# Performance work log

Measured on AMD Instinct MI355X. Metric: run time of the kernel, lower is better.

Reference implementation:

```python
import jax, jax.numpy as jnp
import numpy as np

MIN_NEAR = 0.05
DENSITY_SCALE = 1.0
BOUND = 1.0  # spherical scene bounds radius
GEO = 15


def _density_mlp(x, dW1, db1, dW2, db2, dW3, db3):
    h = jax.nn.relu(x @ dW1 + db1)
    h = jax.nn.relu(h @ dW2 + db2)
    h = h @ dW3 + db3  # [M, 1+GEO]
    sigma = jnp.exp(jnp.clip(h[..., 0], -15.0, 15.0))  # trunc_exp
    return sigma, h[..., 1:]


def _color_mlp(d, geo, cW1, cb1, cW2, cb2, cW3, cb3):
    h = jnp.concatenate([d, geo], axis=-1)
    h = jax.nn.relu(h @ cW1 + cb1)
    h = jax.nn.relu(h @ cW2 + cb2)
    return jax.nn.sigmoid(h @ cW3 + cb3)


def _comp_weights(deltas, sigmas):
    # alpha compositing: w_i = alpha_i * prod_{j<i}(1 - alpha_j)
    alphas = 1.0 - jnp.exp(-deltas * sigmas)
    trans = jnp.cumprod(
        jnp.concatenate([jnp.ones_like(alphas[:, :1]), 1.0 - alphas + 1e-15], axis=-1),
        axis=-1)[:, :-1]
    return alphas * trans


def _sample_pdf(bins, weights, n_samples):
    # deterministic importance resampling (eval mode); bins [N,T-1], weights [N,T-2]
    weights = weights + 1e-5
    pdf = weights / jnp.sum(weights, axis=-1, keepdims=True)
    cdf = jnp.cumsum(pdf, axis=-1)
    cdf = jnp.concatenate([jnp.zeros_like(cdf[:, :1]), cdf], axis=-1)  # [N, T-1]
    u = jnp.linspace(0.5 / n_samples, 1.0 - 0.5 / n_samples, n_samples)
    u = jnp.broadcast_to(u, (bins.shape[0], n_samples))
    inds = jax.vmap(lambda c, uu: jnp.searchsorted(c, uu, side='right'))(cdf, u)
    below = jnp.clip(inds - 1, 0, cdf.shape[-1] - 1)
    above = jnp.clip(inds, 0, cdf.shape[-1] - 1)
    cdf_g0 = jnp.take_along_axis(cdf, below, axis=-1)
    cdf_g1 = jnp.take_along_axis(cdf, above, axis=-1)
    bmax = bins.shape[-1] - 1
    bins_g0 = jnp.take_along_axis(bins, jnp.clip(below, 0, bmax), axis=-1)
    bins_g1 = jnp.take_along_axis(bins, jnp.clip(above, 0, bmax), axis=-1)
    denom = jnp.where(cdf_g1 - cdf_g0 < 1e-5, 1.0, cdf_g1 - cdf_g0)
    t = (u - cdf_g0) / denom
    return bins_g0 + t * (bins_g1 - bins_g0)


def _run(rays_o, rays_d, dW1, db1, dW2, db2, dW3, db3,
         cW1, cb1, cW2, cb2, cW3, cb3, num_steps, upsample_steps):
    N = rays_o.shape[0]
    # get_z_val_bounds: ray/sphere intersection, sphere radius BOUND at origin
    b = jnp.sum(rays_o * rays_d, axis=-1)
    c = jnp.sum(rays_o * rays_o, axis=-1) - BOUND ** 2
    disc = jnp.maximum(b * b - c, 0.0)
    z_max = jnp.maximum(-b + jnp.sqrt(disc), MIN_NEAR + 1e-3)
    z_min = jnp.full_like(z_max, MIN_NEAR)
    # get_foreground_z_vals: per-ray linspace (perturb=False)
    t = jnp.linspace(0.0, 1.0, num_steps)
    z_vals = z_min[:, None] + (z_max - z_min)[:, None] * t[None, :]
    z_vals = jnp.clip(z_vals, z_min[:, None], z_max[:, None])
    xyzs = rays_o[:, None, :] + rays_d[:, None, :] * z_vals[..., None]
    sigma, geo = _density_mlp(xyzs.reshape(-1, 3), dW1, db1, dW2, db2, dW3, db3)
    sigma = sigma.reshape(N, num_steps)
    geo = geo.reshape(N, num_steps, GEO)

    # upsample_z_values: importance resampling from coarse weights
    deltas = z_vals[:, 1:] - z_vals[:, :-1]
    aug = jnp.concatenate([deltas, deltas[:, -1:]], axis=-1)
    w_coarse = _comp_weights(aug, DENSITY_SCALE * sigma)
    z_mid = 0.5 * (z_vals[:, :-1] + z_vals[:, 1:])
    new_z = jax.lax.stop_gradient(_sample_pdf(z_mid, w_coarse[:, 1:-1], upsample_steps))
    new_xyzs = rays_o[:, None, :] + rays_d[:, None, :] * new_z[..., None]
    new_sigma, new_geo = _density_mlp(new_xyzs.reshape(-1, 3), dW1, db1, dW2, db2, dW3, db3)
    new_sigma = new_sigma.reshape(N, upsample_steps)
    new_geo = new_geo.reshape(N, upsample_steps, GEO)

    # sort/gather merge of coarse + fine samples
    z_all = jnp.concatenate([z_vals, new_z], axis=1)
    order = jnp.argsort(z_all, axis=1)
    z_vals = jnp.take_along_axis(z_all, order, axis=1)  # [N, T]
    xyzs = jnp.take_along_axis(jnp.concatenate([xyzs, new_xyzs], axis=1), order[..., None], axis=1)
    sigma = jnp.take_along_axis(jnp.concatenate([sigma, new_sigma], axis=1), order, axis=1)
    geo = jnp.take_along_axis(jnp.concatenate([geo, new_geo], axis=1), order[..., None], axis=1)

    deltas = z_vals[:, 1:] - z_vals[:, :-1]
    aug = jnp.concatenate([deltas, deltas[:, -1:]], axis=-1)
    weights = _comp_weights(aug, DENSITY_SCALE * sigma)  # [N, T]

    mask = weights > 1e-4
    dirs = jnp.broadcast_to(rays_d[:, None, :], xyzs.shape).reshape(-1, 3)
    rgb = _color_mlp(dirs, geo.reshape(-1, GEO), cW1, cb1, cW2, cb2, cW3, cb3)
    rgbs = jnp.where(mask.reshape(-1, 1), rgb, 0.0).reshape(N, -1, 3)

    weights_sum = jnp.sum(weights, axis=-1)
    depth = jnp.sum(weights * z_vals, axis=-1)
    image = jnp.sum(weights[..., None] * rgbs, axis=-2)
    bg = 206.0 / 255.0
    image = image + (1.0 - weights_sum)[..., None] * bg

    # pairwise distortion loss (the (z_shifted - z_shifted) term in the source is identically zero)
    sample_dist = 1.0 / num_steps
    z_shift = jnp.concatenate([z_vals[:, 1:], jnp.full((N, 1), sample_dist, z_vals.dtype)], axis=-1)
    mid_zs = 0.5 * z_vals + 0.5 * z_shift
    pair = jnp.abs(mid_zs[:, None, :] - mid_zs[:, :, None]) * (weights[:, None, :] * weights[:, :, None])
    loss = jnp.sum(pair, axis=(1, 2)) / (depth + 1e-6)
    loss = jnp.where(loss < 1e-3, 0.0, loss)  # cutoff
    return jnp.concatenate([image, depth[:, None], loss[:, None]], axis=-1)  # [N, 5]


def setup_inputs() -> dict:
    key = jax.random.key(0)
    ks = jax.random.split(key, 16)
    N, H = 2048, 256
    rays_o = 0.1 * jax.random.normal(ks[0], (N, 3), jnp.float32)  # near scene centre
    rd = jax.random.normal(ks[1], (N, 3), jnp.float32)
    rays_d = rd / jnp.linalg.norm(rd, axis=-1, keepdims=True)

    def w(k, shape):
        return jax.random.normal(k, shape, jnp.float32) * (1.0 / np.sqrt(shape[0]))

    return {
        'rays_o': rays_o, 'rays_d': rays_d,
        'dW1': w(ks[2], (3, H)), 'db1': jnp.zeros(H, jnp.float32),
        'dW2': w(ks[3], (H, H)), 'db2': jnp.zeros(H, jnp.float32),
        'dW3': w(ks[4], (H, 1 + GEO)), 'db3': jnp.zeros(1 + GEO, jnp.float32),
        'cW1': w(ks[5], (3 + GEO, H)), 'cb1': jnp.zeros(H, jnp.float32),
        'cW2': w(ks[6], (H, H)), 'cb2': jnp.zeros(H, jnp.float32),
        'cW3': w(ks[7], (H, 3)), 'cb3': jnp.zeros(3, jnp.float32),
        'num_steps': 128, 'upsample_steps': 128,
    }


def reference(rays_o, rays_d, dW1, db1, dW2, db2, dW3, db3,
              cW1, cb1, cW2, cb2, cW3, cb3, num_steps, upsample_steps):
    return _run(rays_o, rays_d, dW1, db1, dW2, db2, dW3, db3,
                cW1, cb1, cW2, cb2, cW3, cb3, num_steps, upsample_steps)
```

## Files before the change

### kernel.cpp

```cpp
#include <hip/hip_runtime.h>


typedef float f32x4 __attribute__((ext_vector_type(4)));
typedef __bf16 bf16x8 __attribute__((ext_vector_type(8)));
typedef __bf16 bf16x4 __attribute__((ext_vector_type(4)));
typedef unsigned short u16x8 __attribute__((ext_vector_type(8)));
typedef unsigned short u16x4 __attribute__((ext_vector_type(4)));

#define NRAYS 2048
#define NSTEP 128
#define MIN_NEAR 0.05f

#define OFF_D1 0
#define OFF_D2 8192
#define OFF_D3 73728
#define OFF_C1 77824
#define OFF_C2 86016
#define OFF_C3 151552
#define PACK_TOTAL 155648

__device__ __forceinline__ unsigned short f2bf(float f) {
  __bf16 h = (__bf16)f;
  return __builtin_bit_cast(unsigned short, h);
}
__device__ __forceinline__ u16x4 pack4(float a, float b, float c, float d) {
  bf16x4 h;
  h[0] = (__bf16)a; h[1] = (__bf16)b; h[2] = (__bf16)c; h[3] = (__bf16)d;
  return __builtin_bit_cast(u16x4, h);
}

__device__ __forceinline__ float ray_zmax(const float* __restrict__ ro,
                                          const float* __restrict__ rd, int r) {
  float ox = ro[r * 3], oy = ro[r * 3 + 1], oz = ro[r * 3 + 2];
  float dx = rd[r * 3], dy = rd[r * 3 + 1], dz = rd[r * 3 + 2];
  float b = ox * dx + oy * dy + oz * dz;
  float c = ox * ox + oy * oy + oz * oz - 1.0f;
  float disc = fmaxf(b * b - c, 0.0f);
  return fmaxf(-b + sqrtf(disc), MIN_NEAR + 1e-3f);
}
__device__ __forceinline__ float z_at(float zmax, int i) {
  float zz = MIN_NEAR + (zmax - MIN_NEAR) * ((float)i / 127.0f);
  return fminf(fmaxf(zz, MIN_NEAR), zmax);
}

__device__ __forceinline__ float wave_iscan(float v, int lane) {
#pragma unroll
  for (int off = 1; off < 64; off <<= 1) {
    float y = __shfl_up(v, off, 64);
    if (lane >= off) v += y;
  }
  return v;
}
__device__ __forceinline__ float block_iscan(float v, float* part, int lane, int wid) {
  float s = wave_iscan(v, lane);
  if (lane == 63) part[wid] = s;
  __syncthreads();
  float pre = 0.f;
  if (wid > 0) pre += part[0];
  if (wid > 1) pre += part[1];
  if (wid > 2) pre += part[2];
  return s + pre;
}

__device__ __forceinline__ void pack_std(const float* __restrict__ W,
                                         unsigned short* __restrict__ dst,
                                         int idx, int K, int Norig, int NT) {
  int per = NT * 512;
  int kt = idx / per, rm = idx % per;
  int nt = rm >> 9, lane = (rm >> 3) & 63, j = rm & 7;
  int k = kt * 32 + ((lane >> 4) << 3) + j;
  int n = nt * 16 + (lane & 15);
  float v = (k < K && n < Norig) ? W[k * Norig + n] : 0.0f;
  dst[idx] = f2bf(v);
}

__global__ void k_pack_all(const float* __restrict__ dW1, const float* __restrict__ dW2,
                           const float* __restrict__ dW3, const float* __restrict__ cW1,
                           const float* __restrict__ cW2, const float* __restrict__ cW3,
                           unsigned short* __restrict__ Wp) {
  int idx = blockIdx.x * 256 + threadIdx.x;
  if (idx < OFF_D2) {
    pack_std(dW1, Wp + OFF_D1, idx - OFF_D1, 3, 256, 16);
  } else if (idx < OFF_D3) {
    pack_std(dW2, Wp + OFF_D2, idx - OFF_D2, 256, 256, 16);
  } else if (idx < OFF_C1) {
    int j2 = idx - OFF_D3;
    int lane = (j2 >> 3) & 63, jj = j2 & 7, kt = j2 >> 9;
    int k = kt * 32 + ((lane >> 4) << 3) + jj;
    int n = lane & 15;
    Wp[idx] = f2bf(dW3[k * 16 + ((n + 1) & 15)]);
  } else if (idx < OFF_C2) {
    int j2 = idx - OFF_C1;
    int nt = j2 >> 9, lane = (j2 >> 3) & 63, jj = j2 & 7;
    int k = ((lane >> 4) << 3) + jj;
    int n = nt * 16 + (lane & 15);
    float v = 0.0f;
    if (k < 15) v = cW1[(3 + k) * 256 + n];
    else if (k >= 16 && k < 19) v = cW1[(k - 16) * 256 + n];
    Wp[idx] = f2bf(v);
  } else if (idx < OFF_C3) {
    pack_std(cW2, Wp + OFF_C2, idx - OFF_C2, 256, 256, 16);
  } else if (idx < PACK_TOTAL) {
    pack_std(cW3, Wp + OFF_C3, idx - OFF_C3, 256, 3, 1);
  }
}


__device__ __forceinline__ void mlp_l1(const unsigned short* xb, unsigned short* dst,
                                       const bf16x8 (&w1r)[4], const float* sb1,
                                       int wid, int quad, int col) {
#pragma unroll
  for (int h = 0; h < 2; ++h) {
    f32x4 acc[8];
#pragma unroll
    for (int i = 0; i < 8; ++i) acc[i] = (f32x4){0.f, 0.f, 0.f, 0.f};
    int p0 = (h * 2) * 16 + col, p1 = (h * 2 + 1) * 16 + col;
    bf16x8 x0 = *reinterpret_cast<const bf16x8*>(&xb[p0 * 32 + ((quad ^ (p0 & 3)) * 8)]);
    bf16x8 x1 = *reinterpret_cast<const bf16x8*>(&xb[p1 * 32 + ((quad ^ (p1 & 3)) * 8)]);
#pragma unroll
    for (int ntl = 0; ntl < 4; ++ntl) {
      acc[ntl * 2 + 0] = __builtin_amdgcn_mfma_f32_16x16x32_bf16(w1r[ntl], x0, acc[ntl * 2 + 0], 0, 0, 0);
      acc[ntl * 2 + 1] = __builtin_amdgcn_mfma_f32_16x16x32_bf16(w1r[ntl], x1, acc[ntl * 2 + 1], 0, 0, 0);
    }
#pragma unroll
    for (int ntl = 0; ntl < 4; ++ntl) {
      int n = (wid * 4 + ntl) * 16 + quad * 4;
      f32x4 bv = *reinterpret_cast<const f32x4*>(&sb1[n]);
#pragma unroll
      for (int j = 0; j < 2; ++j) {
        int p = (h * 2 + j) * 16 + col;
        *reinterpret_cast<u16x4*>(&dst[p * 256 + (((n >> 3) ^ (p & 31)) * 8) + (n & 7)]) =
            pack4(fmaxf(acc[ntl * 2 + j][0] + bv[0], 0.f), fmaxf(acc[ntl * 2 + j][1] + bv[1], 0.f),
                  fmaxf(acc[ntl * 2 + j][2] + bv[2], 0.f), fmaxf(acc[ntl * 2 + j][3] + bv[3], 0.f));
      }
    }
  }
}

__device__ __forceinline__ void l2_pass(const unsigned short* src, unsigned short* dst,
                                        const bf16x8 (&w2r)[8][4], const float* sb2,
                                        int h, int wid, int quad, int col) {
  f32x4 acc[8];
#pragma unroll
  for (int i = 0; i < 8; ++i) acc[i] = (f32x4){0.f, 0.f, 0.f, 0.f};
  const int p0 = (h * 2) * 16 + col, p1 = (h * 2 + 1) * 16 + col;
#pragma unroll
  for (int kt = 0; kt < 8; ++kt) {
    bf16x8 x0 = *reinterpret_cast<const bf16x8*>(&src[p0 * 256 + (((kt * 4 + quad) ^ (p0 & 31)) * 8)]);
    bf16x8 x1 = *reinterpret_cast<const bf16x8*>(&src[p1 * 256 + (((kt * 4 + quad) ^ (p1 & 31)) * 8)]);
#pragma unroll
    for (int ntl = 0; ntl < 4; ++ntl) {
      acc[ntl * 2 + 0] = __builtin_amdgcn_mfma_f32_16x16x32_bf16(w2r[kt][ntl], x0, acc[ntl * 2 + 0], 0, 0, 0);
      acc[ntl * 2 + 1] = __builtin_amdgcn_mfma_f32_16x16x32_bf16(w2r[kt][ntl], x1, acc[ntl * 2 + 1], 0, 0, 0);
    }
  }
#pragma unroll
  for (int ntl = 0; ntl < 4; ++ntl) {
    int n = (wid * 4 + ntl) * 16 + quad * 4;
    f32x4 bv = *reinterpret_cast<const f32x4*>(&sb2[n]);
#pragma unroll
    for (int j = 0; j < 2; ++j) {
      int p = (h * 2 + j) * 16 + col;
      *reinterpret_cast<u16x4*>(&dst[p * 256 + (((n >> 3) ^ (p & 31)) * 8) + (n & 7)]) =
          pack4(fmaxf(acc[ntl * 2 + j][0] + bv[0], 0.f), fmaxf(acc[ntl * 2 + j][1] + bv[1], 0.f),
                fmaxf(acc[ntl * 2 + j][2] + bv[2], 0.f), fmaxf(acc[ntl * 2 + j][3] + bv[3], 0.f));
    }
  }
}

template <bool FIRST>
__global__ __launch_bounds__(256, 2)
void k_density(const float* __restrict__ ro, const float* __restrict__ rd,
               const float* __restrict__ zin,
               const unsigned short* __restrict__ Wp1, const float* __restrict__ b1,
               const unsigned short* __restrict__ Wp2, const float* __restrict__ b2,
               const unsigned short* __restrict__ Wp3, const float* __restrict__ b3,
               unsigned short* __restrict__ gout, float* __restrict__ sig,
               float* __restrict__ z_f) {
  __shared__ __align__(16) unsigned short bufA[64 * 256];
  __shared__ __align__(16) unsigned short bufB[64 * 256];
  __shared__ __align__(16) unsigned short xb[64 * 32];
  __shared__ __align__(16) unsigned short sW3[4096];
  __shared__ __align__(16) float sb1[256];
  __shared__ __align__(16) float sb2[256];
  __shared__ __align__(16) float sb3[16];
  __shared__ __align__(16) float ssig[256];
  __shared__ __align__(16) float sred[16];
  const int t = threadIdx.x;
  const int lane = t & 63, wid = t >> 6, quad = lane >> 4, col = lane & 15;
  const int p_ = t >> 2, g_ = t & 3;

  sb1[t] = b1[t];
  sb2[t] = b2[t];
  if (t < 16) sb3[t] = b3[(t + 1) & 15];
  { const u16x8* s = (const u16x8*)Wp3; u16x8* d = (u16x8*)sW3;
    d[t] = s[t]; d[t + 256] = s[t + 256]; }

  bf16x8 w1r[4], w2r[8][4];
#pragma unroll
  for (int ntl = 0; ntl < 4; ++ntl)
    w1r[ntl] = *reinterpret_cast<const bf16x8*>(Wp1 + ((wid * 4 + ntl) * 64 + lane) * 8);
#pragma unroll
  for (int kt = 0; kt < 8; ++kt)
#pragma unroll
    for (int ntl = 0; ntl < 4; ++ntl)
      w2r[kt][ntl] = *reinterpret_cast<const bf16x8*>(Wp2 + ((kt * 16 + wid * 4 + ntl) * 64 + lane) * 8);

  const int rg0 = blockIdx.x * 2;
  float zmax0 = ray_zmax(ro, rd, rg0);
  float zmax1 = ray_zmax(ro, rd, rg0 + 1);
  float oax = ro[rg0 * 3], oay = ro[rg0 * 3 + 1], oaz = ro[rg0 * 3 + 2];
  float dax = rd[rg0 * 3], day = rd[rg0 * 3 + 1], daz = rd[rg0 * 3 + 2];
  float obx = ro[rg0 * 3 + 3], oby = ro[rg0 * 3 + 4], obz = ro[rg0 * 3 + 5];
  float dbx = rd[rg0 * 3 + 3], dby = rd[rg0 * 3 + 4], dbz = rd[rg0 * 3 + 5];
  __syncthreads();

#pragma unroll 1
  for (int tt = 0; tt < 4; ++tt) {
    const int P0 = blockIdx.x * 256 + tt * 64;
    {
      u16x8 pk = {0, 0, 0, 0, 0, 0, 0, 0};
      if (g_ == 0) {
        int P = P0 + p_;
        int hi = (P >> 7) & 1;
        float zz;
        if constexpr (FIRST) zz = z_at(hi ? zmax1 : zmax0, P & 127);
        else zz = zin[P];
        pk[0] = f2bf((hi ? obx : oax) + (hi ? dbx : dax) * zz);
        pk[1] = f2bf((hi ? oby : oay) + (hi ? dby : day) * zz);
        pk[2] = f2bf((hi ? obz : oaz) + (hi ? dbz : daz) * zz);
      }
      *reinterpret_cast<u16x8*>(&xb[p_ * 32 + ((g_ ^ (p_ & 3)) * 8)]) = pk;
    }
    __syncthreads();
    mlp_l1(xb, bufA, w1r, sb1, wid, quad, col);
    __syncthreads();
    l2_pass(bufA, bufB, w2r, sb2, 0, wid, quad, col);
    l2_pass(bufA, bufB, w2r, sb2, 1, wid, quad, col);
    __syncthreads();
    {
      const int p = wid * 16 + col;
      f32x4 a3 = {0.f, 0.f, 0.f, 0.f};
#pragma unroll
      for (int kt = 0; kt < 8; ++kt) {
        bf16x8 w = *reinterpret_cast<const bf16x8*>(&sW3[(kt * 64 + lane) * 8]);
        bf16x8 xx = *reinterpret_cast<const bf16x8*>(&bufB[p * 256 + (((kt * 4 + quad) ^ (p & 31)) * 8)]);
        a3 = __builtin_amdgcn_mfma_f32_16x16x32_bf16(w, xx, a3, 0, 0, 0);
      }
      int n0 = quad * 4;
      float v0 = a3[0] + sb3[n0], v1 = a3[1] + sb3[n0 + 1];
      float v2 = a3[2] + sb3[n0 + 2], v3 = a3[3] + sb3[n0 + 3];
      if (quad == 3) {
        float sgm = __expf(fminf(fmaxf(v3, -15.f), 15.f));
        sig[P0 + p] = sgm;
        if constexpr (FIRST) ssig[tt * 64 + p] = sgm;
        v3 = 0.0f;
      }
      *reinterpret_cast<u16x4*>(gout + (size_t)(P0 + p) * 16 + n0) = pack4(v0, v1, v2, v3);
    }
  }

  if constexpr (FIRST) {
    __syncthreads();
    float* psz = reinterpret_cast<float*>(bufA);
    float* pmid = psz + 256;
    float* pcdf = psz + 512;
    float* psw = psz + 768;
    const int segw = t >> 7;
    const int i = t & 127;
    const int seg = segw * 128;
    float zi = z_at(segw ? zmax1 : zmax0, i);
    psz[seg + i] = zi;
    float sgv = ssig[t];
    __syncthreads();
    float aug = (i < 127) ? psz[seg + i + 1] - zi : psz[seg + 127] - psz[seg + 126];
    float alpha = 1.0f - __expf(-aug * sgv);
    float lt = __logf(1.0f - alpha + 1e-15f);
    float s = wave_iscan(lt, lane);
    if (lane == 63) sred[wid] = s;
    __syncthreads();
    if (wid & 1) s += sred[wid - 1];
    float w = alpha * __expf(s - lt);
    psw[seg + i] = w;
    if (i < 127) pmid[seg + i] = 0.5f * (zi + psz[seg + i + 1]);
    __syncthreads();
    float v2s = (i < 126) ? psw[seg + i + 1] + 1e-5f : 0.f;
    float s2 = wave_iscan(v2s, lane);
    if (lane == 63) sred[8 + wid] = s2;
    __syncthreads();
    if (wid & 1) s2 += sred[8 + wid - 1];
    psw[seg + i] = s2;
    __syncthreads();
    float total = psw[seg + 125];
    if (i <= 126) pcdf[seg + i] = (i == 0) ? 0.f : psw[seg + i - 1] / total;
    __syncthreads();
    const float lo = 0.5f / 128.0f, hi = 1.0f - 0.5f / 128.0f;
    float u = lo + (hi - lo) * ((float)i / 127.0f);
    int loI = 0, hiI = 127;
    while (loI < hiI) {
      int mid = (loI + hiI) >> 1;
      if (pcdf[seg + mid] > u) hiI = mid; else loI = mid + 1;
    }
    int below = loI - 1; if (below < 0) below = 0; if (below > 126) below = 126;
    int above = loI;     if (above > 126) above = 126;
    float c0 = pcdf[seg + below], c1 = pcdf[seg + above];
    float b0v = pmid[seg + below], b1v = pmid[seg + above];
    float dn = c1 - c0; if (dn < 1e-5f) dn = 1.0f;
    float ttt = (u - c0) / dn;
    z_f[(rg0 + segw) * NSTEP + i] = b0v + ttt * (b1v - b0v);
  }
}

__global__ __launch_bounds__(256, 2)
void k_mcf(const float* __restrict__ ro, const float* __restrict__ rd,
           const float* __restrict__ z_f,
           const float* __restrict__ sigc, const float* __restrict__ sigf,
           const unsigned short* __restrict__ goutc, const unsigned short* __restrict__ goutf,
           const unsigned short* __restrict__ Wp1, const float* __restrict__ cb1,
           const unsigned short* __restrict__ Wp2, const float* __restrict__ cb2,
           const unsigned short* __restrict__ Wp3, const float* __restrict__ cb3,
           float* __restrict__ out) {
  __shared__ __align__(16) unsigned short bufA[64 * 256];
  __shared__ __align__(16) unsigned short bufB[64 * 256];
  __shared__ __align__(16) unsigned short xb[64 * 32];
  __shared__ __align__(16) float sb1[256];
  __shared__ __align__(16) float sb2[256];
  __shared__ __align__(16) float szm[256];
  __shared__ __align__(16) float swgt[256];
  __shared__ __align__(16) float srgb[768];
  __shared__ __align__(16) float sred[48];
  __shared__ unsigned short sord[256];
  const int t = threadIdx.x;
  const int lane = t & 63, wid = t >> 6, quad = lane >> 4, col = lane & 15;
  const int p_ = t >> 2, g_ = t & 3;
  const int r = blockIdx.x;

  sb1[t] = cb1[t];
  sb2[t] = cb2[t];

  bf16x8 w1r[4], w2r[8][4];
#pragma unroll
  for (int ntl = 0; ntl < 4; ++ntl)
    w1r[ntl] = *reinterpret_cast<const bf16x8*>(Wp1 + ((wid * 4 + ntl) * 64 + lane) * 8);
#pragma unroll
  for (int kt = 0; kt < 8; ++kt)
#pragma unroll
    for (int ntl = 0; ntl < 4; ++ntl)
      w2r[kt][ntl] = *reinterpret_cast<const bf16x8*>(Wp2 + ((kt * 16 + wid * 4 + ntl) * 64 + lane) * 8);

  float* szc = reinterpret_cast<float*>(bufA);
  float* szf = szc + 128;
  float zmaxr = ray_zmax(ro, rd, r);
  if (t < 128) szc[t] = z_at(zmaxr, t);
  else szf[t - 128] = z_f[r * NSTEP + (t - 128)];
  __syncthreads();
  int pos; float myz;
  if (t < 128) {
    myz = szc[t];
    int lo = 0, hi = 128;
    while (lo < hi) { int m = (lo + hi) >> 1; if (szf[m] < myz) lo = m + 1; else hi = m; }
    pos = t + lo;
  } else {
    int j = t - 128; myz = szf[j];
    int lo = 0, hi = 128;
    while (lo < hi) { int m = (lo + hi) >> 1; if (szc[m] <= myz) lo = m + 1; else hi = m; }
    pos = j + lo;
  }
  szm[pos] = myz; sord[pos] = (unsigned short)t;
  __syncthreads();
  int srci = sord[t];
  float sg = (srci < 128) ? sigc[r * NSTEP + srci] : sigf[r * NSTEP + (srci - 128)];
  float zt = szm[t];
  float aug = (t < 255) ? szm[t + 1] - zt : szm[255] - szm[254];
  float alpha = 1.0f - __expf(-aug * sg);
  float lt = __logf(1.0f - alpha + 1e-15f);
  float incl = block_iscan(lt, sred, lane, wid);
  swgt[t] = alpha * __expf(incl - lt);
  __syncthreads();

  float dv0 = rd[r * 3], dv1 = rd[r * 3 + 1], dv2 = rd[r * 3 + 2];
  u16x8 dirpk = {f2bf(dv0), f2bf(dv1), f2bf(dv2), 0, 0, 0, 0, 0};
  u16x8 gx = {0, 0, 0, 0, 0, 0, 0, 0};
  float wgtv = 0.0f;
  {
    if (g_ < 2) {
      int s0 = sord[p_];
      const unsigned short* gs = ((s0 < 128) ? goutc : goutf)
          + ((size_t)(r * NSTEP + (s0 & 127)) * 16) + g_ * 8;
      gx = *reinterpret_cast<const u16x8*>(gs);
    } else if (g_ == 2) {
      gx = dirpk;
    } else {
      wgtv = swgt[p_];
    }
  }
#pragma unroll 1
  for (int tt = 0; tt < 4; ++tt) {
    const int haveNext = (tt < 3);
    int go = __syncthreads_or((g_ == 3) && (wgtv > 1e-4f));
    int ordn = 0; float wgtn = 0.0f;
    u16x8 gxn = {0, 0, 0, 0, 0, 0, 0, 0};
    if (go) {
      *reinterpret_cast<u16x8*>(&xb[p_ * 32 + ((g_ ^ (p_ & 3)) * 8)]) = gx;
      __syncthreads();
      mlp_l1(xb, bufA, w1r, sb1, wid, quad, col);
      __syncthreads();
    }
    if (haveNext) {
      int Pn = (tt + 1) * 64 + p_;
      if (g_ < 2) ordn = sord[Pn];
      else if (g_ == 2) gxn = dirpk;
      else wgtn = swgt[Pn];
    }
    if (go) {
      l2_pass(bufA, bufB, w2r, sb2, 0, wid, quad, col);
      l2_pass(bufA, bufB, w2r, sb2, 1, wid, quad, col);
    }
    if (haveNext && g_ < 2) {
      const unsigned short* gs = ((ordn < 128) ? goutc : goutf)
          + ((size_t)(r * NSTEP + (ordn & 127)) * 16) + g_ * 8;
      gxn = *reinterpret_cast<const u16x8*>(gs);
    }
    if (go) {
      __syncthreads();
      {
        const int p = wid * 16 + col;
        f32x4 a3 = {0.f, 0.f, 0.f, 0.f};
#pragma unroll
        for (int kt = 0; kt < 8; ++kt) {
          bf16x8 w = *reinterpret_cast<const bf16x8*>(&Wp3[(kt * 64 + lane) * 8]);
          bf16x8 xx = *reinterpret_cast<const bf16x8*>(&bufB[p * 256 + (((kt * 4 + quad) ^ (p & 31)) * 8)]);
          a3 = __builtin_amdgcn_mfma_f32_16x16x32_bf16(w, xx, a3, 0, 0, 0);
        }
        if (quad == 0) {
          int pi = tt * 64 + p;
          srgb[pi * 3 + 0] = 1.0f / (1.0f + __expf(-(a3[0] + cb3[0])));
          srgb[pi * 3 + 1] = 1.0f / (1.0f + __expf(-(a3[1] + cb3[1])));
          srgb[pi * 3 + 2] = 1.0f / (1.0f + __expf(-(a3[2] + cb3[2])));
        }
      }
    }
    gx = gxn; wgtv = wgtn;
  }

  __syncthreads();
  float ztf = szm[t], wtf = swgt[t];
  float znext = (t < 255) ? szm[t + 1] : (1.0f / 128.0f);
  float mt = 0.5f * ztf + 0.5f * znext;
  float cr = 0.f, cg = 0.f, cbl = 0.f;
  if (wtf > 1e-4f) { cr = srgb[t * 3]; cg = srgb[t * 3 + 1]; cbl = srgb[t * 3 + 2]; }
  if (t == 255) { sred[36] = mt; sred[37] = wtf; }
  float wm = (t < 255) ? wtf : 0.f;
  float Pw = block_iscan(wm, sred, lane, wid);
  float Ps = block_iscan(wm * mt, sred + 4, lane, wid);
  float W254 = sred[0] + sred[1] + sred[2] + sred[3];
  float S254 = sred[4] + sred[5] + sred[6] + sred[7];
  float m255 = sred[36], w255 = sred[37];
  float contrib = 0.f;
  if (t < 255)
    contrib = wtf * (mt * (2.f * Pw - W254) - (2.f * Ps - S254))
            + 2.f * wtf * fabsf(mt - m255) * w255;
  float vals[6] = {wtf, wtf * ztf, wtf * cr, wtf * cg, wtf * cbl, contrib};
#pragma unroll
  for (int k = 0; k < 6; ++k) {
    float v = vals[k];
#pragma unroll
    for (int m = 1; m < 64; m <<= 1) v += __shfl_xor(v, m, 64);
    if (lane == 0) sred[8 + k * 4 + wid] = v;
  }
  __syncthreads();
  if (t == 0) {
    float a6[6];
#pragma unroll
    for (int k = 0; k < 6; ++k)
      a6[k] = sred[8 + k * 4] + sred[8 + k * 4 + 1] + sred[8 + k * 4 + 2] + sred[8 + k * 4 + 3];
    const float bgc = 206.0f / 255.0f;
    float wsum = a6[0], depth = a6[1];
    float loss = a6[5] / (depth + 1e-6f);
    if (loss < 1e-3f) loss = 0.0f;
    out[r * 5 + 0] = a6[2] + (1.0f - wsum) * bgc;
    out[r * 5 + 1] = a6[3] + (1.0f - wsum) * bgc;
    out[r * 5 + 2] = a6[4] + (1.0f - wsum) * bgc;
    out[r * 5 + 3] = depth;
    out[r * 5 + 4] = loss;
  }
}

extern "C" void kernel_launch(void* const* d_in, const int* in_sizes, int n_in,
                              void* d_out, int out_size, void* d_ws, size_t ws_size,
                              hipStream_t stream) {
  const float* rays_o = (const float*)d_in[0];
  const float* rays_d = (const float*)d_in[1];
  const float* dW1 = (const float*)d_in[2];
  const float* db1 = (const float*)d_in[3];
  const float* dW2 = (const float*)d_in[4];
  const float* db2 = (const float*)d_in[5];
  const float* dW3 = (const float*)d_in[6];
  const float* db3 = (const float*)d_in[7];
  const float* cW1 = (const float*)d_in[8];
  const float* cb1 = (const float*)d_in[9];
  const float* cW2 = (const float*)d_in[10];
  const float* cb2 = (const float*)d_in[11];
  const float* cW3 = (const float*)d_in[12];
  const float* cb3 = (const float*)d_in[13];

  char* ws = (char*)d_ws;
  size_t off = 0;
  auto alloc = [&](size_t bytes) -> void* {
    void* p = ws + off;
    off += (bytes + 255) & ~(size_t)255;
    return p;
  };
  unsigned short* Wp = (unsigned short*)alloc((size_t)PACK_TOTAL * 2);
  unsigned short* goutc = (unsigned short*)alloc((size_t)NRAYS * NSTEP * 16 * 2);
  unsigned short* goutf = (unsigned short*)alloc((size_t)NRAYS * NSTEP * 16 * 2);
  float* sigc = (float*)alloc((size_t)NRAYS * NSTEP * 4);
  float* sigf = (float*)alloc((size_t)NRAYS * NSTEP * 4);
  float* z_f  = (float*)alloc((size_t)NRAYS * NSTEP * 4);
  (void)ws_size; (void)in_sizes; (void)n_in; (void)out_size;

  k_pack_all<<<PACK_TOTAL / 256, 256, 0, stream>>>(dW1, dW2, dW3, cW1, cW2, cW3, Wp);

  k_density<true><<<(NRAYS * NSTEP) / 256, 256, 0, stream>>>(
      rays_o, rays_d, nullptr,
      Wp + OFF_D1, db1, Wp + OFF_D2, db2, Wp + OFF_D3, db3, goutc, sigc, z_f);
  k_density<false><<<(NRAYS * NSTEP) / 256, 256, 0, stream>>>(
      rays_o, rays_d, z_f,
      Wp + OFF_D1, db1, Wp + OFF_D2, db2, Wp + OFF_D3, db3, goutf, sigf, nullptr);
  k_mcf<<<NRAYS, 256, 0, stream>>>(
      rays_o, rays_d, z_f, sigc, sigf, goutc, goutf,
      Wp + OFF_C1, cb1, Wp + OFF_C2, cb2, Wp + OFF_C3, cb3, (float*)d_out);
}
```

Measured before the change: 325.5 us.

## Share one LDS activation buffer in-place across MLP layers and stage color W3 in LDS

Merges the two 64x256 bf16 LDS activation buffers into one. Layer-2 results are now held in registers and written back in place after an extra barrier per half. The color kernel now copies its final-layer weights into LDS instead of reading them from global memory. Per-ray z bounds are recomputed per sample instead of hoisted. This lowers LDS footprint, which may help occupancy, at the cost of additional __syncthreads and redundant ray loads.

```diff
diff --git a/kernel.cpp b/kernel.cpp
--- a/kernel.cpp
+++ b/kernel.cpp
@@ -29,18 +29,18 @@
   return __builtin_bit_cast(u16x4, h);
 }
 
-__device__ __forceinline__ float ray_zmax(const float* __restrict__ ro,
-                                          const float* __restrict__ rd, int r) {
+__device__ __forceinline__ float ray_z(const float* __restrict__ ro,
+                                       const float* __restrict__ rd, int r, int i) {
   float ox = ro[r * 3], oy = ro[r * 3 + 1], oz = ro[r * 3 + 2];
   float dx = rd[r * 3], dy = rd[r * 3 + 1], dz = rd[r * 3 + 2];
   float b = ox * dx + oy * dy + oz * dz;
   float c = ox * ox + oy * oy + oz * oz - 1.0f;
   float disc = fmaxf(b * b - c, 0.0f);
-  return fmaxf(-b + sqrtf(disc), MIN_NEAR + 1e-3f);
-}
-__device__ __forceinline__ float z_at(float zmax, int i) {
-  float zz = MIN_NEAR + (zmax - MIN_NEAR) * ((float)i / 127.0f);
-  return fminf(fmaxf(zz, MIN_NEAR), zmax);
+  float zmax = fmaxf(-b + sqrtf(disc), MIN_NEAR + 1e-3f);
+  float zmin = MIN_NEAR;
+  float tt = (float)i / 127.0f;
+  float zz = zmin + (zmax - zmin) * tt;
+  return fminf(fmaxf(zz, zmin), zmax);
 }
 
 __device__ __forceinline__ float wave_iscan(float v, int lane) {
@@ -106,7 +106,7 @@
 }
 
 
-__device__ __forceinline__ void mlp_l1(const unsigned short* xb, unsigned short* dst,
+__device__ __forceinline__ void mlp_l1(const unsigned short* xb, unsigned short* buf,
                                        const bf16x8 (&w1r)[4], const float* sb1,
                                        int wid, int quad, int col) {
 #pragma unroll
@@ -129,7 +129,7 @@
 #pragma unroll
       for (int j = 0; j < 2; ++j) {
         int p = (h * 2 + j) * 16 + col;
-        *reinterpret_cast<u16x4*>(&dst[p * 256 + (((n >> 3) ^ (p & 31)) * 8) + (n & 7)]) =
+        *reinterpret_cast<u16x4*>(&buf[p * 256 + (((n >> 3) ^ (p & 31)) * 8) + (n & 7)]) =
             pack4(fmaxf(acc[ntl * 2 + j][0] + bv[0], 0.f), fmaxf(acc[ntl * 2 + j][1] + bv[1], 0.f),
                   fmaxf(acc[ntl * 2 + j][2] + bv[2], 0.f), fmaxf(acc[ntl * 2 + j][3] + bv[3], 0.f));
       }
@@ -137,23 +137,26 @@
   }
 }
 
-__device__ __forceinline__ void l2_pass(const unsigned short* src, unsigned short* dst,
-                                        const bf16x8 (&w2r)[8][4], const float* sb2,
-                                        int h, int wid, int quad, int col) {
-  f32x4 acc[8];
+__device__ __forceinline__ void l2_half_compute(const unsigned short* buf,
+                                                const bf16x8 (&w2r)[8][4],
+                                                f32x4 (&acc)[8], int h, int quad, int col) {
 #pragma unroll
   for (int i = 0; i < 8; ++i) acc[i] = (f32x4){0.f, 0.f, 0.f, 0.f};
-  const int p0 = (h * 2) * 16 + col, p1 = (h * 2 + 1) * 16 + col;
 #pragma unroll
   for (int kt = 0; kt < 8; ++kt) {
-    bf16x8 x0 = *reinterpret_cast<const bf16x8*>(&src[p0 * 256 + (((kt * 4 + quad) ^ (p0 & 31)) * 8)]);
-    bf16x8 x1 = *reinterpret_cast<const bf16x8*>(&src[p1 * 256 + (((kt * 4 + quad) ^ (p1 & 31)) * 8)]);
+    int p0 = (h * 2) * 16 + col, p1 = (h * 2 + 1) * 16 + col;
+    bf16x8 x0 = *reinterpret_cast<const bf16x8*>(&buf[p0 * 256 + (((kt * 4 + quad) ^ (p0 & 31)) * 8)]);
+    bf16x8 x1 = *reinterpret_cast<const bf16x8*>(&buf[p1 * 256 + (((kt * 4 + quad) ^ (p1 & 31)) * 8)]);
 #pragma unroll
     for (int ntl = 0; ntl < 4; ++ntl) {
       acc[ntl * 2 + 0] = __builtin_amdgcn_mfma_f32_16x16x32_bf16(w2r[kt][ntl], x0, acc[ntl * 2 + 0], 0, 0, 0);
       acc[ntl * 2 + 1] = __builtin_amdgcn_mfma_f32_16x16x32_bf16(w2r[kt][ntl], x1, acc[ntl * 2 + 1], 0, 0, 0);
     }
   }
+}
+
+__device__ __forceinline__ void l2_half_write(unsigned short* buf, const f32x4 (&acc)[8],
+                                              const float* sb2, int h, int wid, int quad, int col) {
 #pragma unroll
   for (int ntl = 0; ntl < 4; ++ntl) {
     int n = (wid * 4 + ntl) * 16 + quad * 4;
@@ -161,7 +164,7 @@
 #pragma unroll
     for (int j = 0; j < 2; ++j) {
       int p = (h * 2 + j) * 16 + col;
-      *reinterpret_cast<u16x4*>(&dst[p * 256 + (((n >> 3) ^ (p & 31)) * 8) + (n & 7)]) =
+      *reinterpret_cast<u16x4*>(&buf[p * 256 + (((n >> 3) ^ (p & 31)) * 8) + (n & 7)]) =
           pack4(fmaxf(acc[ntl * 2 + j][0] + bv[0], 0.f), fmaxf(acc[ntl * 2 + j][1] + bv[1], 0.f),
                 fmaxf(acc[ntl * 2 + j][2] + bv[2], 0.f), fmaxf(acc[ntl * 2 + j][3] + bv[3], 0.f));
     }
@@ -177,8 +180,7 @@
                const unsigned short* __restrict__ Wp3, const float* __restrict__ b3,
                unsigned short* __restrict__ gout, float* __restrict__ sig,
                float* __restrict__ z_f) {
-  __shared__ __align__(16) unsigned short bufA[64 * 256];
-  __shared__ __align__(16) unsigned short bufB[64 * 256];
+  __shared__ __align__(16) unsigned short buf[64 * 256];
   __shared__ __align__(16) unsigned short xb[64 * 32];
   __shared__ __align__(16) unsigned short sW3[4096];
   __shared__ __align__(16) float sb1[256];
@@ -206,15 +208,6 @@
     for (int ntl = 0; ntl < 4; ++ntl)
       w2r[kt][ntl] = *reinterpret_cast<const bf16x8*>(Wp2 + ((kt * 16 + wid * 4 + ntl) * 64 + lane) * 8);
 
-  const int rg0 = blockIdx.x * 2;
-  float zmax0 = ray_zmax(ro, rd, rg0);
-  float zmax1 = ray_zmax(ro, rd, rg0 + 1);
-  float oax = ro[rg0 * 3], oay = ro[rg0 * 3 + 1], oaz = ro[rg0 * 3 + 2];
-  float dax = rd[rg0 * 3], day = rd[rg0 * 3 + 1], daz = rd[rg0 * 3 + 2];
-  float obx = ro[rg0 * 3 + 3], oby = ro[rg0 * 3 + 4], obz = ro[rg0 * 3 + 5];
-  float dbx = rd[rg0 * 3 + 3], dby = rd[rg0 * 3 + 4], dbz = rd[rg0 * 3 + 5];
-  __syncthreads();
-
 #pragma unroll 1
   for (int tt = 0; tt < 4; ++tt) {
     const int P0 = blockIdx.x * 256 + tt * 64;
@@ -222,21 +215,26 @@
       u16x8 pk = {0, 0, 0, 0, 0, 0, 0, 0};
       if (g_ == 0) {
         int P = P0 + p_;
-        int hi = (P >> 7) & 1;
+        int rr_ = P >> 7, ii = P & 127;
         float zz;
-        if constexpr (FIRST) zz = z_at(hi ? zmax1 : zmax0, P & 127);
+        if constexpr (FIRST) zz = ray_z(ro, rd, rr_, ii);
         else zz = zin[P];
-        pk[0] = f2bf((hi ? obx : oax) + (hi ? dbx : dax) * zz);
-        pk[1] = f2bf((hi ? oby : oay) + (hi ? dby : day) * zz);
-        pk[2] = f2bf((hi ? obz : oaz) + (hi ? dbz : daz) * zz);
+        pk[0] = f2bf(ro[rr_ * 3 + 0] + rd[rr_ * 3 + 0] * zz);
+        pk[1] = f2bf(ro[rr_ * 3 + 1] + rd[rr_ * 3 + 1] * zz);
+        pk[2] = f2bf(ro[rr_ * 3 + 2] + rd[rr_ * 3 + 2] * zz);
       }
       *reinterpret_cast<u16x8*>(&xb[p_ * 32 + ((g_ ^ (p_ & 3)) * 8)]) = pk;
     }
     __syncthreads();
-    mlp_l1(xb, bufA, w1r, sb1, wid, quad, col);
-    __syncthreads();
-    l2_pass(bufA, bufB, w2r, sb2, 0, wid, quad, col);
-    l2_pass(bufA, bufB, w2r, sb2, 1, wid, quad, col);
+    mlp_l1(xb, buf, w1r, sb1, wid, quad, col);
+    __syncthreads();
+    f32x4 acc[8];
+    l2_half_compute(buf, w2r, acc, 0, quad, col);
+    __syncthreads();
+    l2_half_write(buf, acc, sb2, 0, wid, quad, col);
+    l2_half_compute(buf, w2r, acc, 1, quad, col);
+    __syncthreads();
+    l2_half_write(buf, acc, sb2, 1, wid, quad, col);
     __syncthreads();
     {
       const int p = wid * 16 + col;
@@ -244,7 +242,7 @@
 #pragma unroll
       for (int kt = 0; kt < 8; ++kt) {
         bf16x8 w = *reinterpret_cast<const bf16x8*>(&sW3[(kt * 64 + lane) * 8]);
-        bf16x8 xx = *reinterpret_cast<const bf16x8*>(&bufB[p * 256 + (((kt * 4 + quad) ^ (p & 31)) * 8)]);
+        bf16x8 xx = *reinterpret_cast<const bf16x8*>(&buf[p * 256 + (((kt * 4 + quad) ^ (p & 31)) * 8)]);
         a3 = __builtin_amdgcn_mfma_f32_16x16x32_bf16(w, xx, a3, 0, 0, 0);
       }
       int n0 = quad * 4;
@@ -262,14 +260,15 @@
 
   if constexpr (FIRST) {
     __syncthreads();
-    float* psz = reinterpret_cast<float*>(bufA);
+    float* psz = reinterpret_cast<float*>(buf);
     float* pmid = psz + 256;
     float* pcdf = psz + 512;
     float* psw = psz + 768;
     const int segw = t >> 7;
     const int i = t & 127;
     const int seg = segw * 128;
-    float zi = z_at(segw ? zmax1 : zmax0, i);
+    const int rg = blockIdx.x * 2 + segw;
+    float zi = ray_z(ro, rd, rg, i);
     psz[seg + i] = zi;
     float sgv = ssig[t];
     __syncthreads();
@@ -307,7 +306,7 @@
     float b0v = pmid[seg + below], b1v = pmid[seg + above];
     float dn = c1 - c0; if (dn < 1e-5f) dn = 1.0f;
     float ttt = (u - c0) / dn;
-    z_f[(rg0 + segw) * NSTEP + i] = b0v + ttt * (b1v - b0v);
+    z_f[rg * NSTEP + i] = b0v + ttt * (b1v - b0v);
   }
 }
 
@@ -320,9 +319,9 @@
            const unsigned short* __restrict__ Wp2, const float* __restrict__ cb2,
            const unsigned short* __restrict__ Wp3, const float* __restrict__ cb3,
            float* __restrict__ out) {
-  __shared__ __align__(16) unsigned short bufA[64 * 256];
-  __shared__ __align__(16) unsigned short bufB[64 * 256];
+  __shared__ __align__(16) unsigned short buf[64 * 256];
   __shared__ __align__(16) unsigned short xb[64 * 32];
+  __shared__ __align__(16) unsigned short sW3[4096];
   __shared__ __align__(16) float sb1[256];
   __shared__ __align__(16) float sb2[256];
   __shared__ __align__(16) float szm[256];
@@ -337,6 +336,8 @@
 
   sb1[t] = cb1[t];
   sb2[t] = cb2[t];
+  { const u16x8* s = (const u16x8*)Wp3; u16x8* d = (u16x8*)sW3;
+    d[t] = s[t]; d[t + 256] = s[t + 256]; }
 
   bf16x8 w1r[4], w2r[8][4];
 #pragma unroll
@@ -348,10 +349,9 @@
     for (int ntl = 0; ntl < 4; ++ntl)
       w2r[kt][ntl] = *reinterpret_cast<const bf16x8*>(Wp2 + ((kt * 16 + wid * 4 + ntl) * 64 + lane) * 8);
 
-  float* szc = reinterpret_cast<float*>(bufA);
+  float* szc = reinterpret_cast<float*>(buf);
   float* szf = szc + 128;
-  float zmaxr = ray_zmax(ro, rd, r);
-  if (t < 128) szc[t] = z_at(zmaxr, t);
+  if (t < 128) szc[t] = ray_z(ro, rd, r, t);
   else szf[t - 128] = z_f[r * NSTEP + (t - 128)];
   __syncthreads();
   int pos; float myz;
@@ -403,7 +403,7 @@
     if (go) {
       *reinterpret_cast<u16x8*>(&xb[p_ * 32 + ((g_ ^ (p_ & 3)) * 8)]) = gx;
       __syncthreads();
-      mlp_l1(xb, bufA, w1r, sb1, wid, quad, col);
+      mlp_l1(xb, buf, w1r, sb1, wid, quad, col);
       __syncthreads();
     }
     if (haveNext) {
@@ -412,9 +412,11 @@
       else if (g_ == 2) gxn = dirpk;
       else wgtn = swgt[Pn];
     }
+    f32x4 acc[8];
     if (go) {
-      l2_pass(bufA, bufB, w2r, sb2, 0, wid, quad, col);
-      l2_pass(bufA, bufB, w2r, sb2, 1, wid, quad, col);
+      l2_half_compute(buf, w2r, acc, 0, quad, col);
+      __syncthreads();
+      l2_half_write(buf, acc, sb2, 0, wid, quad, col);
     }
     if (haveNext && g_ < 2) {
       const unsigned short* gs = ((ordn < 128) ? goutc : goutf)
@@ -422,14 +424,17 @@
       gxn = *reinterpret_cast<const u16x8*>(gs);
     }
     if (go) {
+      l2_half_compute(buf, w2r, acc, 1, quad, col);
+      __syncthreads();
+      l2_half_write(buf, acc, sb2, 1, wid, quad, col);
       __syncthreads();
       {
         const int p = wid * 16 + col;
         f32x4 a3 = {0.f, 0.f, 0.f, 0.f};
 #pragma unroll
         for (int kt = 0; kt < 8; ++kt) {
-          bf16x8 w = *reinterpret_cast<const bf16x8*>(&Wp3[(kt * 64 + lane) * 8]);
-          bf16x8 xx = *reinterpret_cast<const bf16x8*>(&bufB[p * 256 + (((kt * 4 + quad) ^ (p & 31)) * 8)]);
+          bf16x8 w = *reinterpret_cast<const bf16x8*>(&sW3[(kt * 64 + lane) * 8]);
+          bf16x8 xx = *reinterpret_cast<const bf16x8*>(&buf[p * 256 + (((kt * 4 + quad) ^ (p & 31)) * 8)]);
           a3 = __builtin_amdgcn_mfma_f32_16x16x32_bf16(w, xx, a3, 0, 0, 0);
         }
         if (quad == 0) {
```

Result: faster. 272.2 us (median of 2 runs) (-16.4%).
